# Kernel optimization log

Measured on AMD Instinct MI355X. Metric: run time of the kernel, lower is better.

## Reference

```python
import jax, jax.numpy as jnp
import numpy as np
from jax import lax

TEMPERATURE = 0.5
MOMENTUM = 0.9
EPS = 1e-12  # F.normalize eps

B, D, K = 8192, 512, 16384


def _l2norm(x):
    # matches F.normalize(p=2): x / max(||x||, eps)
    n = jnp.sqrt(jnp.sum(x * x, axis=-1, keepdims=True))
    return x / jnp.maximum(n, EPS)


def setup_inputs() -> dict:
    key = jax.random.key(0)
    k1, k2, k3 = jax.random.split(key, 3)
    embeddings = jax.random.normal(k1, (B, D), dtype=jnp.float32)
    cluster_ids = jax.random.randint(k2, (B,), 0, K, dtype=jnp.int64)
    prototypes = jax.random.normal(k3, (K, D), dtype=jnp.float32)
    return {"embeddings": embeddings, "cluster_ids": cluster_ids, "prototypes": prototypes}


def reference(embeddings, cluster_ids, prototypes):
    emb_n = _l2norm(embeddings)            # [B, D]
    proto_n = _l2norm(prototypes)          # [K, D]
    sim = jnp.einsum('bd,kd->bk', emb_n, proto_n) / TEMPERATURE  # [B, K]

    pos = jnp.take_along_axis(sim, cluster_ids[:, None], axis=1)  # [B, 1]
    # mask out the positive column, then stable logsumexp over negatives
    is_pos = jnp.arange(sim.shape[1])[None, :] == cluster_ids[:, None]  # [B, K]
    neg = jnp.where(is_pos, -jnp.inf, sim)
    lse = jax.scipy.special.logsumexp(neg, axis=1, keepdims=True)       # [B, 1]
    loss = jnp.mean(-pos + lse)

    # serial momentum EMA update (order-dependent for duplicate cluster ids)
    def step(protos, xc):
        x, c = xc
        row = MOMENTUM * protos[c] + (1.0 - MOMENTUM) * x
        return protos.at[c].set(row), None

    new_protos, _ = lax.scan(step, prototypes, (embeddings, cluster_ids))
    return loss, new_protos
```

## Files before the change

kernel.cpp:

```cpp
#include <hip/hip_runtime.h>
#include <hip/hip_bf16.h>


#define B_N 8192
#define D_N 512
#define K_N 16384
#define INV_T 2.0f
#define MOM 0.9f

#define BM 128
#define BKF 128
#define BTR 128
#define KSPLIT 8
#define NTILE 16
#define BUFB 16384
#define CAP 64

typedef __attribute__((ext_vector_type(8))) int intx8;
typedef __attribute__((ext_vector_type(4))) float floatx4;

__device__ __forceinline__ void gl_lds16(const void* g, void* lds) {
    __builtin_amdgcn_global_load_lds(
        (const __attribute__((address_space(1))) void*)g,
        (__attribute__((address_space(3))) void*)lds, 16, 0, 0);
}

__device__ __forceinline__ intx8 frag2(const unsigned char* rp, int o0, int o1) {
    intx8 v;
    ((int4*)&v)[0] = *(const int4*)(rp + o0);
    ((int4*)&v)[1] = *(const int4*)(rp + o1);
    return v;
}

__device__ __forceinline__ floatx4 mxfma(intx8 a, intx8 b, floatx4 c) {
    return __builtin_amdgcn_mfma_scale_f32_16x16x128_f8f6f4(a, b, c, 0, 0, 0,
                                                            0x7F7F7F7F, 0, 0x7F7F7F7F);
}

__global__ void norm_kernel(const float* __restrict__ emb, const float* __restrict__ pro,
                            unsigned char* __restrict__ embq, unsigned char* __restrict__ proq,
                            float* __restrict__ rowsum, float* __restrict__ out) {
    if (blockIdx.x < 32) rowsum[blockIdx.x * 256 + threadIdx.x] = 0.0f;
    if (blockIdx.x == 32 && threadIdx.x == 0) out[0] = 0.0f;
    int row = blockIdx.x * 4 + (threadIdx.x >> 6);
    int lane = threadIdx.x & 63;
    const float* x;
    unsigned char* o;
    if (row < B_N) {
        x = emb + (size_t)row * D_N;
        o = embq + (size_t)row * D_N;
    } else {
        x = pro + (size_t)(row - B_N) * D_N;
        o = proq + (size_t)(row - B_N) * D_N;
    }
    const float4* xp = (const float4*)(x + lane * 8);
    float4 v0 = xp[0];
    float4 v1 = xp[1];
    float ss = v0.x * v0.x + v0.y * v0.y + v0.z * v0.z + v0.w * v0.w +
               v1.x * v1.x + v1.y * v1.y + v1.z * v1.z + v1.w * v1.w;
    #pragma unroll
    for (int of = 32; of; of >>= 1) ss += __shfl_xor(ss, of);
    float sc = 16.0f / fmaxf(sqrtf(ss), 1e-12f);
    int w0 = 0, w1 = 0;
    w0 = __builtin_amdgcn_cvt_pk_fp8_f32(v0.x * sc, v0.y * sc, w0, false);
    w0 = __builtin_amdgcn_cvt_pk_fp8_f32(v0.z * sc, v0.w * sc, w0, true);
    w1 = __builtin_amdgcn_cvt_pk_fp8_f32(v1.x * sc, v1.y * sc, w1, false);
    w1 = __builtin_amdgcn_cvt_pk_fp8_f32(v1.z * sc, v1.w * sc, w1, true);
    int2 st = {w0, w1};
    *(int2*)(o + lane * 8) = st;
}

__global__ void pos_kernel(const float* __restrict__ emb, const float* __restrict__ pro,
                           const int* __restrict__ cid, float* __restrict__ rowpos) {
    int b = blockIdx.x * 4 + (threadIdx.x >> 6);
    int lane = threadIdx.x & 63;
    int c = cid[b];
    const float4* ep = (const float4*)(emb + (size_t)b * D_N + lane * 8);
    const float4* pp = (const float4*)(pro + (size_t)c * D_N + lane * 8);
    float4 e0 = ep[0], e1 = ep[1], p0 = pp[0], p1 = pp[1];
    float dp = e0.x * p0.x + e0.y * p0.y + e0.z * p0.z + e0.w * p0.w +
               e1.x * p1.x + e1.y * p1.y + e1.z * p1.z + e1.w * p1.w;
    float ee = e0.x * e0.x + e0.y * e0.y + e0.z * e0.z + e0.w * e0.w +
               e1.x * e1.x + e1.y * e1.y + e1.z * e1.z + e1.w * e1.w;
    float qq = p0.x * p0.x + p0.y * p0.y + p0.z * p0.z + p0.w * p0.w +
               p1.x * p1.x + p1.y * p1.y + p1.z * p1.z + p1.w * p1.w;
    #pragma unroll
    for (int o = 32; o; o >>= 1) {
        dp += __shfl_xor(dp, o);
        ee += __shfl_xor(ee, o);
        qq += __shfl_xor(qq, o);
    }
    if (lane == 0)
        rowpos[b] = INV_T * dp / (fmaxf(sqrtf(ee), 1e-12f) * fmaxf(sqrtf(qq), 1e-12f));
}

#define FSTEP(CH)                                                                     \
    do {                                                                              \
        const int cc = tt * 4 + (CH);                                                 \
        if (cc + 1 < NTILE * 4) {         \
            const unsigned char* s = bS + (size_t)(((cc + 1) >> 2) * BTR) * D_N +     \
                                     ((((CH) + 1) & 3) << 7);                         \
            unsigned char* d = Bs + ((cc + 1) & 1) * BUFB + w * 1024;                 \
            _Pragma("unroll")                                                         \
            for (int p = 0; p < 4; p++)                                               \
                gl_lds16(s + (size_t)p * 32 * D_N, d + p * 4096);                     \
        }                                                                             \
        const unsigned char* rb = Bs + ((cc)&1) * BUFB + (wn * 64 + lcol) * BKF;      \
        intx8 bfA0 = frag2(rb + 0 * (16 * BKF), fsw0, fsw1);                          \
        intx8 bfA1 = frag2(rb + 1 * (16 * BKF), fsw0, fsw1);                          \
        __builtin_amdgcn_s_setprio(1);                                                \
        _Pragma("unroll")                                                             \
        for (int i = 0; i < 4; i++) {                                                 \
            acc[i][0] = mxfma(afr[(CH)][i], bfA0, acc[i][0]);                         \
            acc[i][1] = mxfma(afr[(CH)][i], bfA1, acc[i][1]);                         \
        }                                                                             \
        __builtin_amdgcn_s_setprio(0);                                                \
        intx8 bfB0 = frag2(rb + 2 * (16 * BKF), fsw0, fsw1);                          \
        intx8 bfB1 = frag2(rb + 3 * (16 * BKF), fsw0, fsw1);                          \
        __builtin_amdgcn_s_setprio(1);                                                \
        _Pragma("unroll")                                                             \
        for (int i = 0; i < 4; i++) {                                                 \
            acc[i][2] = mxfma(afr[(CH)][i], bfB0, acc[i][2]);                         \
            acc[i][3] = mxfma(afr[(CH)][i], bfB1, acc[i][3]);                         \
        }                                                                             \
        __builtin_amdgcn_s_setprio(0);                                                \
        if ((CH) == 3) {     \
            _Pragma("unroll")                                                         \
            for (int i = 0; i < 4; i++)                                               \
                _Pragma("unroll")                                                     \
                for (int j = 0; j < 4; j++)                                           \
                    _Pragma("unroll")                                                 \
                    for (int r = 0; r < 4; r++) {                                     \
                        rs[i * 4 + r] += __expf(acc[i][j][r] * (INV_T / 256.0f));     \
                        acc[i][j][r] = 0.0f;                                          \
                    }                                                                 \
        }                                                                             \
        __syncthreads();   \
    } while (0)

__global__ __launch_bounds__(256, 2) void flash_kernel(const unsigned char* __restrict__ embq,
                                                       const unsigned char* __restrict__ proq,
                                                       float* __restrict__ rowsum_g) {
    __shared__ __align__(16) unsigned char Bs[2 * BUFB];
    const int t = threadIdx.x;
    const int w = t >> 6, lane = t & 63;
    const int quad = lane >> 4, lcol = lane & 15;
    const int wm = w >> 1, wn = w & 1;

    const int wgl = blockIdx.x;
    const int ks = wgl & 7;
    const int bxp = wgl >> 3;
    const int rowBase = bxp * BM;
    const int kb = ks * (K_N / KSPLIT);

    const int fsw0 = (((quad << 1) | 0) ^ (lcol & 7)) << 4;
    const int fsw1 = (((quad << 1) | 1) ^ (lcol & 7)) << 4;

    const unsigned char* bS = proq + (size_t)(kb + w * 8 + (lane >> 3)) * D_N +
                              (((lane & 7) ^ ((lane >> 3) & 7)) << 4);

    floatx4 acc[4][4];
    float rs[16];
    #pragma unroll
    for (int i = 0; i < 4; i++)
        #pragma unroll
        for (int j = 0; j < 4; j++) {
            floatx4 z = {0.0f, 0.0f, 0.0f, 0.0f};
            acc[i][j] = z;
        }
    #pragma unroll
    for (int i = 0; i < 16; i++) rs[i] = 0.0f;

    intx8 afr[4][4];
    {
        const unsigned char* aBase =
            embq + (size_t)(rowBase + wm * 64 + lcol) * D_N + quad * 32;
        #pragma unroll
        for (int ch = 0; ch < 4; ch++)
            #pragma unroll
            for (int i = 0; i < 4; i++) {
                const unsigned char* p = aBase + (size_t)i * (16 * D_N) + (ch << 7);
                ((int4*)&afr[ch][i])[0] = *(const int4*)(p);
                ((int4*)&afr[ch][i])[1] = *(const int4*)(p + 16);
            }
    }
    #pragma unroll
    for (int p = 0; p < 4; p++)
        gl_lds16(bS + (size_t)p * 32 * D_N, Bs + p * 4096 + w * 1024);
    __syncthreads();

    for (int tt = 0; tt < NTILE; tt++) {
        FSTEP(0);
        FSTEP(1);
        FSTEP(2);
        FSTEP(3);
    }

    #pragma unroll
    for (int i = 0; i < 16; i++) {
        #pragma unroll
        for (int o = 1; o < 16; o <<= 1) rs[i] += __shfl_xor(rs[i], o);
    }
    if (lcol == 0) {
        #pragma unroll
        for (int i = 0; i < 4; i++)
            #pragma unroll
            for (int r = 0; r < 4; r++)
                atomicAdd(&rowsum_g[rowBase + wm * 64 + i * 16 + quad * 4 + r],
                          rs[i * 4 + r]);
    }
}

__global__ void loss_kernel(const float* __restrict__ rowsum, const float* __restrict__ rowpos,
                            float* __restrict__ out, int* __restrict__ cnt) {
    __shared__ float red[256];
    int t = threadIdx.x;
    int b = blockIdx.x * 256 + t;
    cnt[b * 2] = 0;
    cnt[b * 2 + 1] = 0;
    float p = rowpos[b];
    red[t] = logf(rowsum[b] - __expf(p)) - p;
    __syncthreads();
    for (int o = 128; o; o >>= 1) {
        if (t < o) red[t] += red[t + o];
        __syncthreads();
    }
    if (t == 0) atomicAdd(out, red[0] * (1.0f / (float)B_N));
}

__global__ void ema_count(const int* __restrict__ cid, int* __restrict__ cnt,
                          int* __restrict__ bucket) {
    int b = blockIdx.x * 256 + threadIdx.x;
    int c = cid[b];
    int slot = atomicAdd(&cnt[c], 1);
    if (slot < CAP) bucket[c * CAP + slot] = b;
}

__global__ void ema_apply(const float* __restrict__ emb, const float* __restrict__ pro,
                          const int* __restrict__ cnt, const int* __restrict__ bucket,
                          float* __restrict__ outp) {
    int k = blockIdx.x * 4 + (threadIdx.x >> 6);
    int lane = threadIdx.x & 63;
    int n = cnt[k];
    n = n < CAP ? n : CAP;
    const float4* pp = (const float4*)(pro + (size_t)k * D_N + lane * 8);
    float4 a0 = pp[0], a1 = pp[1];
    int myb = (lane < n) ? bucket[k * CAP + lane] : 0x7fffffff;
    for (int i = 0; i < n; i++) {
        int m = myb;
        #pragma unroll
        for (int o = 1; o < 64; o <<= 1) {
            int v = __shfl_xor(m, o);
            m = v < m ? v : m;
        }
        const float4* ep = (const float4*)(emb + (size_t)m * D_N + lane * 8);
        float4 e0 = ep[0], e1 = ep[1];
        a0.x = MOM * a0.x + (1.0f - MOM) * e0.x;
        a0.y = MOM * a0.y + (1.0f - MOM) * e0.y;
        a0.z = MOM * a0.z + (1.0f - MOM) * e0.z;
        a0.w = MOM * a0.w + (1.0f - MOM) * e0.w;
        a1.x = MOM * a1.x + (1.0f - MOM) * e1.x;
        a1.y = MOM * a1.y + (1.0f - MOM) * e1.y;
        a1.z = MOM * a1.z + (1.0f - MOM) * e1.z;
        a1.w = MOM * a1.w + (1.0f - MOM) * e1.w;
        if (myb == m) myb = 0x7fffffff;
    }
    float4* op = (float4*)(outp + (size_t)k * D_N + lane * 8);
    op[0] = a0;
    op[1] = a1;
}

extern "C" void kernel_launch(void* const* d_in, const int* in_sizes, int n_in,
                              void* d_out, int out_size, void* d_ws, size_t ws_size,
                              hipStream_t stream) {
    const float* emb = (const float*)d_in[0];
    const int* cid = (const int*)d_in[1];
    const float* pro = (const float*)d_in[2];
    float* out = (float*)d_out;

    char* ws = (char*)d_ws;
    unsigned char* embq = (unsigned char*)ws;
    unsigned char* proq = (unsigned char*)(ws + 4194304);
    float* rowsum = (float*)(ws + 12582912);
    float* rowpos = (float*)(ws + 12615680);
    int* cnt = (int*)(ws + 4194304);
    int* bucket = (int*)(ws + 4194304 + 65536);

    norm_kernel<<<(B_N + K_N) / 4, 256, 0, stream>>>(emb, pro, embq, proq, rowsum, out);
    pos_kernel<<<B_N / 4, 256, 0, stream>>>(emb, pro, cid, rowpos);
    flash_kernel<<<dim3(64 * KSPLIT), 256, 0, stream>>>(embq, proq, rowsum);
    loss_kernel<<<B_N / 256, 256, 0, stream>>>(rowsum, rowpos, out, cnt);
    ema_count<<<B_N / 256, 256, 0, stream>>>(cid, cnt, bucket);
    ema_apply<<<K_N / 4, 256, 0, stream>>>(emb, pro, cnt, bucket, out + 1);
}
```

Baseline: 190.9 us.

## Restructure flash kernel to smaller per-wave tiles with full-depth B tiles and higher occupancy

Reorganizes the fp8 MFMA logsumexp kernel so each wave owns 32 rows against a 32-prototype tile with full 512 depth per step, instead of 64x64 per wave with K-chunked staging. Accumulators and A fragments shrink, which allows launch bounds of 4 workgroups per CU instead of 2. The exp reduction now happens every step over fewer values. The trade-off is less register-level reuse of B fragments across waves, since every wave reads the whole B tile, plus more barriers per unit of work.

```diff
diff --git a/kernel.cpp b/kernel.cpp
--- a/kernel.cpp
+++ b/kernel.cpp
@@ -9,10 +9,8 @@
 #define MOM 0.9f
 
 #define BM 128
-#define BKF 128
-#define BTR 128
 #define KSPLIT 8
-#define NTILE 16
+#define NSTEP 64
 #define BUFB 16384
 #define CAP 64
 
@@ -94,120 +92,96 @@
         rowpos[b] = INV_T * dp / (fmaxf(sqrtf(ee), 1e-12f) * fmaxf(sqrtf(qq), 1e-12f));
 }
 
-#define FSTEP(CH)                                                                     \
-    do {                                                                              \
-        const int cc = tt * 4 + (CH);                                                 \
-        if (cc + 1 < NTILE * 4) {         \
-            const unsigned char* s = bS + (size_t)(((cc + 1) >> 2) * BTR) * D_N +     \
-                                     ((((CH) + 1) & 3) << 7);                         \
-            unsigned char* d = Bs + ((cc + 1) & 1) * BUFB + w * 1024;                 \
-            _Pragma("unroll")                                                         \
-            for (int p = 0; p < 4; p++)                                               \
-                gl_lds16(s + (size_t)p * 32 * D_N, d + p * 4096);                     \
-        }                                                                             \
-        const unsigned char* rb = Bs + ((cc)&1) * BUFB + (wn * 64 + lcol) * BKF;      \
-        intx8 bfA0 = frag2(rb + 0 * (16 * BKF), fsw0, fsw1);                          \
-        intx8 bfA1 = frag2(rb + 1 * (16 * BKF), fsw0, fsw1);                          \
-        __builtin_amdgcn_s_setprio(1);                                                \
-        _Pragma("unroll")                                                             \
-        for (int i = 0; i < 4; i++) {                                                 \
-            acc[i][0] = mxfma(afr[(CH)][i], bfA0, acc[i][0]);                         \
-            acc[i][1] = mxfma(afr[(CH)][i], bfA1, acc[i][1]);                         \
-        }                                                                             \
-        __builtin_amdgcn_s_setprio(0);                                                \
-        intx8 bfB0 = frag2(rb + 2 * (16 * BKF), fsw0, fsw1);                          \
-        intx8 bfB1 = frag2(rb + 3 * (16 * BKF), fsw0, fsw1);                          \
-        __builtin_amdgcn_s_setprio(1);                                                \
-        _Pragma("unroll")                                                             \
-        for (int i = 0; i < 4; i++) {                                                 \
-            acc[i][2] = mxfma(afr[(CH)][i], bfB0, acc[i][2]);                         \
-            acc[i][3] = mxfma(afr[(CH)][i], bfB1, acc[i][3]);                         \
-        }                                                                             \
-        __builtin_amdgcn_s_setprio(0);                                                \
-        if ((CH) == 3) {     \
-            _Pragma("unroll")                                                         \
-            for (int i = 0; i < 4; i++)                                               \
-                _Pragma("unroll")                                                     \
-                for (int j = 0; j < 4; j++)                                           \
-                    _Pragma("unroll")                                                 \
-                    for (int r = 0; r < 4; r++) {                                     \
-                        rs[i * 4 + r] += __expf(acc[i][j][r] * (INV_T / 256.0f));     \
-                        acc[i][j][r] = 0.0f;                                          \
-                    }                                                                 \
-        }                                                                             \
-        __syncthreads();   \
-    } while (0)
-
-__global__ __launch_bounds__(256, 2) void flash_kernel(const unsigned char* __restrict__ embq,
+__global__ __launch_bounds__(256, 4) void flash_kernel(const unsigned char* __restrict__ embq,
                                                        const unsigned char* __restrict__ proq,
                                                        float* __restrict__ rowsum_g) {
     __shared__ __align__(16) unsigned char Bs[2 * BUFB];
     const int t = threadIdx.x;
     const int w = t >> 6, lane = t & 63;
     const int quad = lane >> 4, lcol = lane & 15;
-    const int wm = w >> 1, wn = w & 1;
 
     const int wgl = blockIdx.x;
     const int ks = wgl & 7;
-    const int bxp = wgl >> 3;
-    const int rowBase = bxp * BM;
+    const int rowBase = (wgl >> 3) * BM;
     const int kb = ks * (K_N / KSPLIT);
 
     const int fsw0 = (((quad << 1) | 0) ^ (lcol & 7)) << 4;
     const int fsw1 = (((quad << 1) | 1) ^ (lcol & 7)) << 4;
 
-    const unsigned char* bS = proq + (size_t)(kb + w * 8 + (lane >> 3)) * D_N +
-                              (((lane & 7) ^ ((lane >> 3) & 7)) << 4);
-
-    floatx4 acc[4][4];
-    float rs[16];
-    #pragma unroll
-    for (int i = 0; i < 4; i++)
-        #pragma unroll
-        for (int j = 0; j < 4; j++) {
-            floatx4 z = {0.0f, 0.0f, 0.0f, 0.0f};
-            acc[i][j] = z;
-        }
-    #pragma unroll
-    for (int i = 0; i < 16; i++) rs[i] = 0.0f;
-
-    intx8 afr[4][4];
+    const int srow = w * 2 + (lane >> 5);
+    const int g = lane & 31;
+    const unsigned char* bS = proq + (size_t)(kb + srow) * D_N + ((g >> 3) << 7) +
+                              (((g & 7) ^ (srow & 7)) << 4);
+
+    float rs[8];
+    #pragma unroll
+    for (int i = 0; i < 8; i++) rs[i] = 0.0f;
+
+    intx8 afr[4][2];
     {
         const unsigned char* aBase =
-            embq + (size_t)(rowBase + wm * 64 + lcol) * D_N + quad * 32;
+            embq + (size_t)(rowBase + w * 32 + lcol) * D_N + quad * 32;
         #pragma unroll
         for (int ch = 0; ch < 4; ch++)
             #pragma unroll
-            for (int i = 0; i < 4; i++) {
-                const unsigned char* p = aBase + (size_t)i * (16 * D_N) + (ch << 7);
-                ((int4*)&afr[ch][i])[0] = *(const int4*)(p);
-                ((int4*)&afr[ch][i])[1] = *(const int4*)(p + 16);
+            for (int mi = 0; mi < 2; mi++) {
+                const unsigned char* p = aBase + (size_t)mi * (16 * D_N) + (ch << 7);
+                ((int4*)&afr[ch][mi])[0] = *(const int4*)(p);
+                ((int4*)&afr[ch][mi])[1] = *(const int4*)(p + 16);
             }
     }
     #pragma unroll
     for (int p = 0; p < 4; p++)
-        gl_lds16(bS + (size_t)p * 32 * D_N, Bs + p * 4096 + w * 1024);
+        gl_lds16(bS + (size_t)p * 8 * D_N, Bs + p * 4096 + w * 1024);
     __syncthreads();
 
-    for (int tt = 0; tt < NTILE; tt++) {
-        FSTEP(0);
-        FSTEP(1);
-        FSTEP(2);
-        FSTEP(3);
-    }
-
-    #pragma unroll
-    for (int i = 0; i < 16; i++) {
+    const unsigned char* bSrc = bS + (size_t)32 * D_N;
+    for (int s = 0; s < NSTEP; s++) {
+        if (s + 1 < NSTEP) {
+            unsigned char* d = Bs + ((s + 1) & 1) * BUFB + w * 1024;
+            #pragma unroll
+            for (int p = 0; p < 4; p++)
+                gl_lds16(bSrc + (size_t)p * 8 * D_N, d + p * 4096);
+        }
+        bSrc += (size_t)32 * D_N;
+
+        const unsigned char* rb0 = Bs + (s & 1) * BUFB + lcol * 512;
+        const unsigned char* rb1 = rb0 + 16 * 512;
+        floatx4 a00 = {0.f, 0.f, 0.f, 0.f}, a01 = {0.f, 0.f, 0.f, 0.f};
+        floatx4 a10 = {0.f, 0.f, 0.f, 0.f}, a11 = {0.f, 0.f, 0.f, 0.f};
+        __builtin_amdgcn_s_setprio(1);
+        #pragma unroll
+        for (int ch = 0; ch < 4; ch++) {
+            intx8 b0 = frag2(rb0 + (ch << 7), fsw0, fsw1);
+            intx8 b1 = frag2(rb1 + (ch << 7), fsw0, fsw1);
+            a00 = mxfma(afr[ch][0], b0, a00);
+            a01 = mxfma(afr[ch][0], b1, a01);
+            a10 = mxfma(afr[ch][1], b0, a10);
+            a11 = mxfma(afr[ch][1], b1, a11);
+        }
+        __builtin_amdgcn_s_setprio(0);
+
+        #pragma unroll
+        for (int r = 0; r < 4; r++) {
+            rs[r] += __expf(a00[r] * (INV_T / 256.0f)) + __expf(a01[r] * (INV_T / 256.0f));
+            rs[4 + r] += __expf(a10[r] * (INV_T / 256.0f)) + __expf(a11[r] * (INV_T / 256.0f));
+        }
+
+        __syncthreads();
+    }
+
+    #pragma unroll
+    for (int i = 0; i < 8; i++) {
         #pragma unroll
         for (int o = 1; o < 16; o <<= 1) rs[i] += __shfl_xor(rs[i], o);
     }
     if (lcol == 0) {
         #pragma unroll
-        for (int i = 0; i < 4; i++)
+        for (int mi = 0; mi < 2; mi++)
             #pragma unroll
             for (int r = 0; r < 4; r++)
-                atomicAdd(&rowsum_g[rowBase + wm * 64 + i * 16 + quad * 4 + r],
-                          rs[i * 4 + r]);
+                atomicAdd(&rowsum_g[rowBase + w * 32 + mi * 16 + quad * 4 + r],
+                          rs[mi * 4 + r]);
     }
 }
 
```

After: 198.4 us. 3.9% more time.
